# Performance work log

Hardware: AMD Instinct MI355X
Metric: run time of the kernel (lower is better)

The kernel has to match this reference:

```python
import jax, jax.numpy as jnp
import numpy as np

B, S, D = 4, 2048, 1024
H, DH = 16, 64  # dim_q = dim_k = D // H
DFF = 4096


def setup_inputs() -> dict:
    key = jax.random.key(0)
    ks = jax.random.split(key, 12)
    sd = 0.02
    x = jax.random.normal(ks[0], (B, S, D), dtype=jnp.float32)
    mask = jax.random.randint(ks[1], (B, S, S), 0, 2) == 1  # True = masked
    Wq = jax.random.normal(ks[2], (H, D, DH), dtype=jnp.float32) * sd
    bq = jnp.zeros((H, DH), dtype=jnp.float32)
    Wk = jax.random.normal(ks[3], (H, D, DH), dtype=jnp.float32) * sd
    bk = jnp.zeros((H, DH), dtype=jnp.float32)
    Wv = jax.random.normal(ks[4], (H, D, DH), dtype=jnp.float32) * sd
    bv = jnp.zeros((H, DH), dtype=jnp.float32)
    Wo = jax.random.normal(ks[5], (H * DH, D), dtype=jnp.float32) * sd
    bo = jnp.zeros((D,), dtype=jnp.float32)
    W1 = jax.random.normal(ks[6], (D, DFF), dtype=jnp.float32) * sd
    b1 = jnp.zeros((DFF,), dtype=jnp.float32)
    W2 = jax.random.normal(ks[7], (DFF, D), dtype=jnp.float32) * sd
    b2 = jnp.zeros((D,), dtype=jnp.float32)
    return dict(x=x, mask=mask, Wq=Wq, bq=bq, Wk=Wk, bk=bk, Wv=Wv, bv=bv,
                Wo=Wo, bo=bo, W1=W1, b1=b1, W2=W2, b2=b2)


def reference(x, mask, Wq, bq, Wk, bk, Wv, bv, Wo, bo, W1, b1, W2, b2):
    # x: [B,S,D]; mask: [B,S,S] bool (True -> masked)
    # Per-head projections, batched over heads: [B,H,S,DH]
    q = jnp.einsum('bsd,hde->bhse', x, Wq) + bq[None, :, None, :]
    k = jnp.einsum('bsd,hde->bhse', x, Wk) + bk[None, :, None, :]
    v = jnp.einsum('bsd,hde->bhse', x, Wv) + bv[None, :, None, :]
    # NOTE: source scales by sqrt(seq_len) (query.size(1)), reproduced faithfully.
    scale = x.shape[1] ** 0.5
    scores = jnp.einsum('bhse,bhte->bhst', q, k) / scale  # [B,H,S,S]
    scores = jnp.where(mask[:, None, :, :], -1e9, scores)
    attn = jax.nn.softmax(scores, axis=-1)
    ctx = jnp.einsum('bhst,bhte->bhse', attn, v)  # [B,H,S,DH]
    # concat heads -> [B,S,H*DH], output projection
    ctx = jnp.transpose(ctx, (0, 2, 1, 3)).reshape(x.shape[0], x.shape[1], -1)
    out = ctx @ Wo + bo
    # FFN (no residual/LayerNorm in source; dropout = identity in eval)
    h = jax.nn.relu(out @ W1 + b1)
    return h @ W2 + b2
```

## Files before the change

### kernel.cpp

```cpp
#include <hip/hip_runtime.h>
#include <hip/hip_bf16.h>


#define SDIM 2048
#define DDIM 1024

using floatx4 = __attribute__((ext_vector_type(4))) float;
using bf16x8  = __attribute__((ext_vector_type(8))) __bf16;
using bf16x4  = __attribute__((ext_vector_type(4))) __bf16;
using short4v = __attribute__((ext_vector_type(4))) short;

#define GLDS16(gptr, lptr)                                                        \
    __builtin_amdgcn_global_load_lds(                                             \
        (const __attribute__((address_space(1))) void*)(uintptr_t)(gptr),         \
        (__attribute__((address_space(3))) void*)(uintptr_t)(lptr), 16, 0, 0)


__global__ void k_f2b(const float* __restrict__ in, __bf16* __restrict__ out) {
    long i = ((long)blockIdx.x * 256 + threadIdx.x) * 4;
    float4 f = *(const float4*)(in + i);
    bf16x4 v;
    v[0] = (__bf16)f.x; v[1] = (__bf16)f.y; v[2] = (__bf16)f.z; v[3] = (__bf16)f.w;
    *(bf16x4*)(out + i) = v;
}

__global__ void k_tr(const float* __restrict__ in, __bf16* __restrict__ out, int R, int C) {
    __shared__ float t[32][33];
    int nrt = R >> 5;
    int tr = blockIdx.x % nrt, tc = blockIdx.x / nrt;
    int r0 = tr * 32, c0 = tc * 32;
    int lx = threadIdx.x & 31, ly = threadIdx.x >> 5;
    #pragma unroll
    for (int i = 0; i < 32; i += 8) t[ly + i][lx] = in[(long)(r0 + ly + i) * C + c0 + lx];
    __syncthreads();
    #pragma unroll
    for (int i = 0; i < 32; i += 8) out[(long)(c0 + ly + i) * R + r0 + lx] = (__bf16)t[lx][ly + i];
}

__global__ void k_pack_qkvw(const float* __restrict__ Wq, const float* __restrict__ Wk,
                            const float* __restrict__ Wv, __bf16* __restrict__ out) {
    int bid = blockIdx.x;
    int dht = bid & 1;
    int dt = (bid >> 1) & 31;
    int h = (bid >> 6) & 15;
    int which = bid >> 10;
    const float* W = (which == 0) ? Wq : (which == 1) ? Wk : Wv;
    __shared__ float t[32][33];
    int lx = threadIdx.x & 31, ly = threadIdx.x >> 5;
    const float* src = W + ((long)h * 1024 + dt * 32) * 64 + dht * 32;
    #pragma unroll
    for (int i = 0; i < 32; i += 8) t[ly + i][lx] = src[(ly + i) * 64 + lx];
    __syncthreads();
    __bf16* dst = out + ((long)(which * 1024 + h * 64 + dht * 32)) * 1024 + dt * 32;
    #pragma unroll
    for (int i = 0; i < 32; i += 8) dst[(long)(ly + i) * 1024 + lx] = (__bf16)t[lx][ly + i];
}

__global__ void k_pack_qkvb(const float* bq, const float* bk, const float* bv, float* out) {
    int i = blockIdx.x * 256 + threadIdx.x;
    if (i < 3072) {
        int which = i >> 10, r = i & 1023;
        const float* s = (which == 0) ? bq : (which == 1) ? bk : bv;
        out[i] = s[r];
    }
}

__global__ void k_probe(const unsigned* __restrict__ m, int* flag) {
    __shared__ int bad;
    if (threadIdx.x == 0) bad = 0;
    __syncthreads();
    int local = 0;
    for (int i = 0; i < 64; i++) {
        unsigned w = m[threadIdx.x + 256 * i];
        if (w != 0u && w != 1u && w != 0x3f800000u) local = 1;
    }
    if (local) atomicOr(&bad, 1);
    __syncthreads();
    if (threadIdx.x == 0) *flag = bad ? 0 : 1;
}

__global__ void k_pack_mask(const void* __restrict__ mask, const int* __restrict__ flag,
                            unsigned long long* __restrict__ bits) {
    long wid = ((long)blockIdx.x * 256 + threadIdx.x) >> 6;
    int lane = threadIdx.x & 63;
    long e = wid * 64 + lane;
    bool pred;
    if (*flag) pred = ((const unsigned*)mask)[e] != 0u;
    else       pred = ((const unsigned char*)mask)[e] != 0;
    unsigned long long bal = __ballot(pred);
    if (lane == 0) bits[wid] = bal;
}

__global__ void k_remap(const unsigned* __restrict__ bitsDW, unsigned* __restrict__ out) {
    int t = blockIdx.x * 256 + threadIdx.x;
    int q = t & 3, kt = (t >> 2) & 15, srow = t >> 6;
    uint4 md = *(const uint4*)(bitsDW + (long)srow * 64 + kt * 4);
    unsigned d[4] = {md.x, md.y, md.z, md.w};
    unsigned acc = 0;
    #pragma unroll
    for (int ct = 0; ct < 8; ct++) {
        unsigned nib = (d[ct >> 1] >> (((ct & 1) << 4) + q * 4)) & 0xFu;
        acc |= nib << (ct * 4);
    }
    out[t] = acc;
}

__global__ void k_trv(const __bf16* __restrict__ Vrow, __bf16* __restrict__ Vt) {
    __shared__ __bf16 t[32][72];
    int p = blockIdx.x >> 6, ts = blockIdx.x & 63;
    int tid = threadIdx.x;
    const __bf16* src = Vrow + ((long)p * 2048 + ts * 32) * 64;
    int s = tid >> 3, c = (tid & 7) * 8;
    *(bf16x8*)&t[s][c] = *(const bf16x8*)&src[s * 64 + c];
    __syncthreads();
    int dh = tid >> 2, sb = (tid & 3) * 8;
    bf16x8 w;
    #pragma unroll
    for (int j = 0; j < 8; j++) w[j] = t[sb + j][dh];
    *(bf16x8*)&Vt[((long)p * 64 + dh) * 2048 + ts * 32 + sb] = w;
}

#define QSZ 8388608L

template <int MODE>
__global__ __launch_bounds__(256, 4) void k_gemm(const __bf16* __restrict__ A,
                                                 const __bf16* __restrict__ Bt,
                                                 const float* __restrict__ bias,
                                                 void* __restrict__ Cout, int Ndim, int K) {
    __shared__ __align__(16) __bf16 As[128 * 64];
    __shared__ __align__(16) __bf16 Bs[128 * 64];
    const int tid = threadIdx.x;
    const int wave = tid >> 6, lane = tid & 63;
    const int q = lane >> 4, l16 = lane & 15;
    const int wr = wave >> 1, wc = wave & 1;
    const long bm = (long)blockIdx.x * 128;
    const long bn = (long)blockIdx.y * 128;
    floatx4 acc[4][4] = {};

    const int srow = lane >> 3;
    const int scol = (((lane & 7) - srow) & 7) * 8;
    const int r8 = l16 & 7;

    const char* apA0 = (const char*)As + (wr * 64 + l16) * 128 + ((q + r8) & 7) * 16;
    const char* apA1 = (const char*)As + (wr * 64 + l16) * 128 + ((q + 4 + r8) & 7) * 16;
    const char* apB0 = (const char*)Bs + (wc * 64 + l16) * 128 + ((q + r8) & 7) * 16;
    const char* apB1 = (const char*)Bs + (wc * 64 + l16) * 128 + ((q + 4 + r8) & 7) * 16;

    for (int k0 = 0; k0 < K; k0 += 64) {
        __syncthreads();
        #pragma unroll
        for (int c = 0; c < 4; c++) {
            int row0 = wave * 32 + c * 8;
            GLDS16(&A[(bm + row0 + srow) * K + k0 + scol], (char*)As + row0 * 128);
            GLDS16(&Bt[(bn + row0 + srow) * K + k0 + scol], (char*)Bs + row0 * 128);
        }
        __syncthreads();
        bf16x8 af[4], bfr[4];
        #pragma unroll
        for (int i = 0; i < 4; i++) af[i] = *(const bf16x8*)(apA0 + i * 2048);
        #pragma unroll
        for (int j = 0; j < 4; j++) bfr[j] = *(const bf16x8*)(apB0 + j * 2048);
        #pragma unroll
        for (int i = 0; i < 4; i++)
            #pragma unroll
            for (int j = 0; j < 4; j++)
                acc[i][j] = __builtin_amdgcn_mfma_f32_16x16x32_bf16(af[i], bfr[j], acc[i][j], 0, 0, 0);
        #pragma unroll
        for (int i = 0; i < 4; i++) af[i] = *(const bf16x8*)(apA1 + i * 2048);
        #pragma unroll
        for (int j = 0; j < 4; j++) bfr[j] = *(const bf16x8*)(apB1 + j * 2048);
        #pragma unroll
        for (int i = 0; i < 4; i++)
            #pragma unroll
            for (int j = 0; j < 4; j++)
                acc[i][j] = __builtin_amdgcn_mfma_f32_16x16x32_bf16(af[i], bfr[j], acc[i][j], 0, 0, 0);
    }

    const int mrow0 = (int)bm + wr * 64 + q * 4;
    const int ncol0 = (int)bn + wc * 64;
    #pragma unroll
    for (int j = 0; j < 4; j++) {
        int nbase = ncol0 + j * 16 + l16;
        float bv = bias[nbase];
        #pragma unroll
        for (int i = 0; i < 4; i++) {
            #pragma unroll
            for (int r = 0; r < 4; r++) {
                int mm = mrow0 + i * 16 + r;
                float v = acc[i][j][r] + bv;
                if (MODE == 2) v = fmaxf(v, 0.f);
                if (MODE == 3) {
                    ((float*)Cout)[(long)mm * Ndim + nbase] = v;
                } else if (MODE == 0) {
                    int which = nbase >> 10, rem = nbase & 1023;
                    int hh = rem >> 6, dh = rem & 63;
                    int bb = mm >> 11, ss = mm & 2047;
                    long pr = (long)(bb * 16 + hh);
                    __bf16* o = (__bf16*)Cout;
                    if (which == 0) {
                        v *= 0.03188152837f;
                        o[(pr * 2048 + ss) * 64 + dh] = (__bf16)v;
                    } else if (which == 1) o[QSZ + (pr * 2048 + ss) * 64 + dh] = (__bf16)v;
                    else o[3 * QSZ + (pr * 2048 + ss) * 64 + dh] = (__bf16)v;
                } else {
                    ((__bf16*)Cout)[(long)mm * Ndim + nbase] = (__bf16)v;
                }
            }
        }
    }
}

__global__ __launch_bounds__(256, 3) void k_attn(const __bf16* __restrict__ Q,
                                                 const __bf16* __restrict__ Kb,
                                                 const __bf16* __restrict__ Vt,
                                                 const unsigned* __restrict__ bitw2,
                                                 __bf16* __restrict__ ctx) {
    __shared__ __align__(16) __bf16 Qs[128 * 64];
    __shared__ __align__(16) __bf16 Ks[128 * 64];
    __shared__ __align__(16) __bf16 Vts[64 * 128];
    const int tid = threadIdx.x, wave = tid >> 6, lane = tid & 63;
    const int q = lane >> 4, l16 = lane & 15;
    const int pair = blockIdx.x & 63, qt = blockIdx.x >> 6;
    const int b = pair >> 4, h = pair & 15;

    const int srow8 = lane >> 3;
    const int scol8 = (((lane & 7) - srow8) & 7) * 8;
    const int r8 = l16 & 7;
    const int vrow = lane >> 4;
    const int vl = lane & 15;

    const __bf16* Qp = Q + ((long)pair * SDIM + qt * 128) * 64;
    #pragma unroll
    for (int c = 0; c < 4; c++) {
        int row0 = wave * 32 + c * 8;
        GLDS16(&Qp[(row0 + srow8) * 64 + scol8], (char*)Qs + row0 * 128);
    }
    __syncthreads();
    bf16x8 qf[2][2];
    #pragma unroll
    for (int g = 0; g < 2; g++) {
        const char* qb = (const char*)Qs + (wave * 32 + g * 16 + l16) * 128;
        qf[g][0] = *(const bf16x8*)(qb + ((q + r8) & 7) * 16);
        qf[g][1] = *(const bf16x8*)(qb + ((q + 4 + r8) & 7) * 16);
    }

    const char* kp0 = (const char*)Ks + l16 * 128 + ((q + r8) & 7) * 16;
    const char* kp1 = (const char*)Ks + l16 * 128 + ((q + 4 + r8) & 7) * 16;
    const char* vp[8];
    #pragma unroll
    for (int ct = 0; ct < 8; ct++)
        vp[ct] = (const char*)Vts + l16 * 256 + (q & 1) * 8 + ((ct * 2 + (q >> 1) + l16) & 15) * 16;
    const int qrow = qt * 128 + wave * 32 + l16;
    const unsigned* mp0 = bitw2 + ((long)(b * SDIM + qrow)) * 64 + q;
    const unsigned* mp1 = mp0 + 16 * 64;

    floatx4 o[2][4] = {};
    floatx4 o5[2] = {};
    short4v ones;
    { union { unsigned u[2]; short4v s; } c; c.u[0] = 0x3F803F80u; c.u[1] = 0x3F803F80u; ones = c.s; }

    for (int kt = 0; kt < 16; kt++) {
        __syncthreads();
        const __bf16* Kp = Kb + ((long)pair * SDIM + kt * 128) * 64;
        #pragma unroll
        for (int c = 0; c < 4; c++) {
            int row0 = wave * 32 + c * 8;
            GLDS16(&Kp[(row0 + srow8) * 64 + scol8], (char*)Ks + row0 * 128);
        }
        const __bf16* Vp = Vt + ((long)pair * 64) * SDIM + kt * 128;
        #pragma unroll
        for (int c = 0; c < 4; c++) {
            int row0 = wave * 16 + c * 4;
            int gsrc = ((vl - (c * 4 + vrow)) & 15) * 8;
            GLDS16(&Vp[(long)(row0 + vrow) * SDIM + gsrc], (char*)Vts + row0 * 256);
        }
        const unsigned w32a = mp0[kt * 4];
        const unsigned w32b = mp1[kt * 4];
        __syncthreads();

        __builtin_amdgcn_s_setprio(1);
        floatx4 st0[8], st1[8];
        #pragma unroll
        for (int ct = 0; ct < 8; ct++) {
            bf16x8 kf0 = *(const bf16x8*)(kp0 + ct * 2048);
            bf16x8 kf1 = *(const bf16x8*)(kp1 + ct * 2048);
            floatx4 z0 = {}, z1 = {};
            z0 = __builtin_amdgcn_mfma_f32_16x16x32_bf16(kf0, qf[0][0], z0, 0, 0, 0);
            z1 = __builtin_amdgcn_mfma_f32_16x16x32_bf16(kf0, qf[1][0], z1, 0, 0, 0);
            z0 = __builtin_amdgcn_mfma_f32_16x16x32_bf16(kf1, qf[0][1], z0, 0, 0, 0);
            z1 = __builtin_amdgcn_mfma_f32_16x16x32_bf16(kf1, qf[1][1], z1, 0, 0, 0);
            st0[ct] = z0; st1[ct] = z1;
        }
        #pragma unroll
        for (int ct = 0; ct < 8; ct++) {
            union { unsigned u[2]; short4v s; } pu0, pu1;
            {
                float p0 = __builtin_amdgcn_exp2f(st0[ct][0]);
                float p1 = __builtin_amdgcn_exp2f(st0[ct][1]);
                float p2 = __builtin_amdgcn_exp2f(st0[ct][2]);
                float p3 = __builtin_amdgcn_exp2f(st0[ct][3]);
                p0 = (w32a & (1u << (ct * 4 + 0))) ? 0.f : p0;
                p1 = (w32a & (1u << (ct * 4 + 1))) ? 0.f : p1;
                p2 = (w32a & (1u << (ct * 4 + 2))) ? 0.f : p2;
                p3 = (w32a & (1u << (ct * 4 + 3))) ? 0.f : p3;
                union { float f; unsigned u; } c0, c1, c2, c3;
                c0.f = p0; c1.f = p1; c2.f = p2; c3.f = p3;
                pu0.u[0] = __builtin_amdgcn_perm(c1.u, c0.u, 0x07060302u);
                pu0.u[1] = __builtin_amdgcn_perm(c3.u, c2.u, 0x07060302u);
            }
            {
                float p0 = __builtin_amdgcn_exp2f(st1[ct][0]);
                float p1 = __builtin_amdgcn_exp2f(st1[ct][1]);
                float p2 = __builtin_amdgcn_exp2f(st1[ct][2]);
                float p3 = __builtin_amdgcn_exp2f(st1[ct][3]);
                p0 = (w32b & (1u << (ct * 4 + 0))) ? 0.f : p0;
                p1 = (w32b & (1u << (ct * 4 + 1))) ? 0.f : p1;
                p2 = (w32b & (1u << (ct * 4 + 2))) ? 0.f : p2;
                p3 = (w32b & (1u << (ct * 4 + 3))) ? 0.f : p3;
                union { float f; unsigned u; } c0, c1, c2, c3;
                c0.f = p0; c1.f = p1; c2.f = p2; c3.f = p3;
                pu1.u[0] = __builtin_amdgcn_perm(c1.u, c0.u, 0x07060302u);
                pu1.u[1] = __builtin_amdgcn_perm(c3.u, c2.u, 0x07060302u);
            }
            #pragma unroll
            for (int d = 0; d < 4; d++) {
                union { bf16x4 b; short4v s; } vu;
                vu.b = *(const bf16x4*)(vp[ct] + d * 4096);
                o[0][d] = __builtin_amdgcn_mfma_f32_16x16x16bf16_1k(vu.s, pu0.s, o[0][d], 0, 0, 0);
                o[1][d] = __builtin_amdgcn_mfma_f32_16x16x16bf16_1k(vu.s, pu1.s, o[1][d], 0, 0, 0);
            }
            o5[0] = __builtin_amdgcn_mfma_f32_16x16x16bf16_1k(ones, pu0.s, o5[0], 0, 0, 0);
            o5[1] = __builtin_amdgcn_mfma_f32_16x16x16bf16_1k(ones, pu1.s, o5[1], 0, 0, 0);
        }
        __builtin_amdgcn_s_setprio(0);
    }
    #pragma unroll
    for (int g = 0; g < 2; g++) {
        float inv = 1.0f / o5[g][0];
        long base = ((long)b * SDIM + qrow + g * 16) * DDIM + h * 64;
        #pragma unroll
        for (int d = 0; d < 4; d++) {
            bf16x4 w;
            #pragma unroll
            for (int r = 0; r < 4; r++) w[r] = (__bf16)(o[g][d][r] * inv);
            *(bf16x4*)&ctx[base + d * 16 + q * 4] = w;
        }
    }
}


extern "C" void kernel_launch(void* const* d_in, const int* in_sizes, int n_in,
                              void* d_out, int out_size, void* d_ws, size_t ws_size,
                              hipStream_t stream) {
    const float* x = (const float*)d_in[0];
    const void* mask = d_in[1];
    const float* Wq = (const float*)d_in[2];
    const float* bq = (const float*)d_in[3];
    const float* Wk = (const float*)d_in[4];
    const float* bk = (const float*)d_in[5];
    const float* Wv = (const float*)d_in[6];
    const float* bv = (const float*)d_in[7];
    const float* Wo = (const float*)d_in[8];
    const float* bo = (const float*)d_in[9];
    const float* W1 = (const float*)d_in[10];
    const float* b1 = (const float*)d_in[11];
    const float* W2 = (const float*)d_in[12];
    const float* b2 = (const float*)d_in[13];

    char* ws = (char*)d_ws;
    __bf16* xb   = (__bf16*)(ws + 0);
    __bf16* Qb   = (__bf16*)(ws + 16777216);
    __bf16* Kb   = (__bf16*)(ws + 33554432);
    __bf16* Vtb  = (__bf16*)(ws + 50331648);
    __bf16* Vrow = (__bf16*)(ws + 67108864);
    __bf16* hbuf = (__bf16*)(ws + 33554432);
    __bf16* wqkvt = (__bf16*)(ws + 100663296);
    __bf16* wot  = (__bf16*)(ws + 106954752);
    __bf16* w1t  = (__bf16*)(ws + 109051904);
    __bf16* w2t  = (__bf16*)(ws + 117440512);
    float* bqkv  = (float*)(ws + 125829120);
    int* flag    = (int*)(ws + 125841408);
    __bf16* ctx = xb;
    __bf16* attn_out = Qb;
    unsigned long long* bits = (unsigned long long*)wqkvt;
    unsigned* bits2 = (unsigned*)((char*)wqkvt + 2097152);
    (void)Vrow;

    k_f2b<<<8192, 256, 0, stream>>>(x, xb);
    k_pack_qkvw<<<3072, 256, 0, stream>>>(Wq, Wk, Wv, wqkvt);
    k_pack_qkvb<<<12, 256, 0, stream>>>(bq, bk, bv, bqkv);
    k_tr<<<1024, 256, 0, stream>>>(Wo, wot, 1024, 1024);
    k_tr<<<4096, 256, 0, stream>>>(W1, w1t, 1024, 4096);
    k_tr<<<4096, 256, 0, stream>>>(W2, w2t, 4096, 1024);
    k_probe<<<1, 256, 0, stream>>>((const unsigned*)mask, flag);

    {
        dim3 g(64, 24);
        k_gemm<0><<<g, 256, 0, stream>>>(xb, wqkvt, bqkv, (void*)Qb, 3072, 1024);
    }
    k_trv<<<4096, 256, 0, stream>>>(Vrow, Vtb);
    k_pack_mask<<<65536, 256, 0, stream>>>(mask, flag, bits);
    k_remap<<<2048, 256, 0, stream>>>((const unsigned*)bits, bits2);
    k_attn<<<1024, 256, 0, stream>>>(Qb, Kb, Vtb, bits2, ctx);
    {
        dim3 g(64, 8);
        k_gemm<1><<<g, 256, 0, stream>>>(ctx, wot, bo, (void*)attn_out, 1024, 1024);
    }
    {
        dim3 g(64, 32);
        k_gemm<2><<<g, 256, 0, stream>>>(attn_out, w1t, b1, (void*)hbuf, 4096, 1024);
    }
    {
        dim3 g(64, 8);
        k_gemm<3><<<g, 256, 0, stream>>>(hbuf, w2t, b2, d_out, 1024, 4096);
    }
}
```

Measured before the change: 595.7 us.

## Double-buffer K/V tiles in attention kernel to overlap loads with compute

The attention kernel now uses two LDS buffers for K and V^T and prefetches the next key tile while computing on the current one. Explicit vmcnt waits and barriers replace the per-iteration syncthreads pairs. The mask bitword layout is remapped so each lane reads contiguous words indexed by kt. Launch bounds drop from 3 to 2 blocks per CU because LDS use grows, which trades occupancy for load/compute overlap.

```diff
diff --git a/kernel.cpp b/kernel.cpp
--- a/kernel.cpp
+++ b/kernel.cpp
@@ -102,7 +102,7 @@
         unsigned nib = (d[ct >> 1] >> (((ct & 1) << 4) + q * 4)) & 0xFu;
         acc |= nib << (ct * 4);
     }
-    out[t] = acc;
+    out[srow * 64 + q * 16 + kt] = acc;
 }
 
 __global__ void k_trv(const __bf16* __restrict__ Vrow, __bf16* __restrict__ Vt) {
@@ -210,14 +210,14 @@
     }
 }
 
-__global__ __launch_bounds__(256, 3) void k_attn(const __bf16* __restrict__ Q,
+__global__ __launch_bounds__(256, 2) void k_attn(const __bf16* __restrict__ Q,
                                                  const __bf16* __restrict__ Kb,
                                                  const __bf16* __restrict__ Vt,
                                                  const unsigned* __restrict__ bitw2,
                                                  __bf16* __restrict__ ctx) {
     __shared__ __align__(16) __bf16 Qs[128 * 64];
-    __shared__ __align__(16) __bf16 Ks[128 * 64];
-    __shared__ __align__(16) __bf16 Vts[64 * 128];
+    __shared__ __align__(16) __bf16 Ks[2][128 * 64];
+    __shared__ __align__(16) __bf16 Vts[2][64 * 128];
     const int tid = threadIdx.x, wave = tid >> 6, lane = tid & 63;
     const int q = lane >> 4, l16 = lane & 15;
     const int pair = blockIdx.x & 63, qt = blockIdx.x >> 6;
@@ -229,13 +229,47 @@
     const int vrow = lane >> 4;
     const int vl = lane & 15;
 
+    const char* kp0 = (const char*)Ks + l16 * 128 + ((q + r8) & 7) * 16;
+    const char* kp1 = (const char*)Ks + l16 * 128 + ((q + 4 + r8) & 7) * 16;
+    const char* vp[8];
+    #pragma unroll
+    for (int ct = 0; ct < 8; ct++)
+        vp[ct] = (const char*)Vts + l16 * 256 + (q & 1) * 8 + ((ct * 2 + (q >> 1) + l16) & 15) * 16;
+    const int qrow = qt * 128 + wave * 32 + l16;
+    const unsigned* mp0 = bitw2 + ((long)(b * SDIM + qrow)) * 64 + q * 16;
+    const unsigned* mp1 = mp0 + 16 * 64;
+
+    floatx4 o[2][4] = {};
+    floatx4 o5[2] = {};
+    short4v ones;
+    { union { unsigned u[2]; short4v s; } c; c.u[0] = 0x3F803F80u; c.u[1] = 0x3F803F80u; ones = c.s; }
+
+    auto stage_kv = [&](int kt, int bufsel) __attribute__((always_inline)) {
+        const __bf16* Kp = Kb + ((long)pair * SDIM + kt * 128) * 64;
+        #pragma unroll
+        for (int c = 0; c < 4; c++) {
+            int row0 = wave * 32 + c * 8;
+            GLDS16(&Kp[(row0 + srow8) * 64 + scol8], (char*)Ks + bufsel * 16384 + row0 * 128);
+        }
+        const __bf16* Vp = Vt + ((long)pair * 64) * SDIM + kt * 128;
+        #pragma unroll
+        for (int c = 0; c < 4; c++) {
+            int row0 = wave * 16 + c * 4;
+            int gsrc = ((vl - (c * 4 + vrow)) & 15) * 8;
+            GLDS16(&Vp[(long)(row0 + vrow) * SDIM + gsrc], (char*)Vts + bufsel * 16384 + row0 * 256);
+        }
+    };
+
     const __bf16* Qp = Q + ((long)pair * SDIM + qt * 128) * 64;
     #pragma unroll
     for (int c = 0; c < 4; c++) {
         int row0 = wave * 32 + c * 8;
         GLDS16(&Qp[(row0 + srow8) * 64 + scol8], (char*)Qs + row0 * 128);
     }
-    __syncthreads();
+    unsigned waA = mp0[0], wbA = mp1[0];
+    stage_kv(0, 0);
+    asm volatile("s_waitcnt vmcnt(8)\n\ts_barrier" ::: "memory");
+
     bf16x8 qf[2][2];
     #pragma unroll
     for (int g = 0; g < 2; g++) {
@@ -244,46 +278,13 @@
         qf[g][1] = *(const bf16x8*)(qb + ((q + 4 + r8) & 7) * 16);
     }
 
-    const char* kp0 = (const char*)Ks + l16 * 128 + ((q + r8) & 7) * 16;
-    const char* kp1 = (const char*)Ks + l16 * 128 + ((q + 4 + r8) & 7) * 16;
-    const char* vp[8];
-    #pragma unroll
-    for (int ct = 0; ct < 8; ct++)
-        vp[ct] = (const char*)Vts + l16 * 256 + (q & 1) * 8 + ((ct * 2 + (q >> 1) + l16) & 15) * 16;
-    const int qrow = qt * 128 + wave * 32 + l16;
-    const unsigned* mp0 = bitw2 + ((long)(b * SDIM + qrow)) * 64 + q;
-    const unsigned* mp1 = mp0 + 16 * 64;
-
-    floatx4 o[2][4] = {};
-    floatx4 o5[2] = {};
-    short4v ones;
-    { union { unsigned u[2]; short4v s; } c; c.u[0] = 0x3F803F80u; c.u[1] = 0x3F803F80u; ones = c.s; }
-
-    for (int kt = 0; kt < 16; kt++) {
-        __syncthreads();
-        const __bf16* Kp = Kb + ((long)pair * SDIM + kt * 128) * 64;
-        #pragma unroll
-        for (int c = 0; c < 4; c++) {
-            int row0 = wave * 32 + c * 8;
-            GLDS16(&Kp[(row0 + srow8) * 64 + scol8], (char*)Ks + row0 * 128);
-        }
-        const __bf16* Vp = Vt + ((long)pair * 64) * SDIM + kt * 128;
-        #pragma unroll
-        for (int c = 0; c < 4; c++) {
-            int row0 = wave * 16 + c * 4;
-            int gsrc = ((vl - (c * 4 + vrow)) & 15) * 8;
-            GLDS16(&Vp[(long)(row0 + vrow) * SDIM + gsrc], (char*)Vts + row0 * 256);
-        }
-        const unsigned w32a = mp0[kt * 4];
-        const unsigned w32b = mp1[kt * 4];
-        __syncthreads();
-
+    auto compute = [&](int off, unsigned w32a, unsigned w32b) __attribute__((always_inline)) {
         __builtin_amdgcn_s_setprio(1);
         floatx4 st0[8], st1[8];
         #pragma unroll
         for (int ct = 0; ct < 8; ct++) {
-            bf16x8 kf0 = *(const bf16x8*)(kp0 + ct * 2048);
-            bf16x8 kf1 = *(const bf16x8*)(kp1 + ct * 2048);
+            bf16x8 kf0 = *(const bf16x8*)(kp0 + off + ct * 2048);
+            bf16x8 kf1 = *(const bf16x8*)(kp1 + off + ct * 2048);
             floatx4 z0 = {}, z1 = {};
             z0 = __builtin_amdgcn_mfma_f32_16x16x32_bf16(kf0, qf[0][0], z0, 0, 0, 0);
             z1 = __builtin_amdgcn_mfma_f32_16x16x32_bf16(kf0, qf[1][0], z1, 0, 0, 0);
@@ -325,7 +326,7 @@
             #pragma unroll
             for (int d = 0; d < 4; d++) {
                 union { bf16x4 b; short4v s; } vu;
-                vu.b = *(const bf16x4*)(vp[ct] + d * 4096);
+                vu.b = *(const bf16x4*)(vp[ct] + off + d * 4096);
                 o[0][d] = __builtin_amdgcn_mfma_f32_16x16x16bf16_1k(vu.s, pu0.s, o[0][d], 0, 0, 0);
                 o[1][d] = __builtin_amdgcn_mfma_f32_16x16x16bf16_1k(vu.s, pu1.s, o[1][d], 0, 0, 0);
             }
@@ -333,7 +334,31 @@
             o5[1] = __builtin_amdgcn_mfma_f32_16x16x16bf16_1k(ones, pu1.s, o5[1], 0, 0, 0);
         }
         __builtin_amdgcn_s_setprio(0);
-    }
+    };
+
+    #pragma unroll 1
+    for (int kt = 0; kt < 14; kt += 2) {
+        unsigned waB = mp0[kt + 1], wbB = mp1[kt + 1];
+        stage_kv(kt + 1, 1);
+        asm volatile("s_waitcnt vmcnt(10)\n\ts_barrier" ::: "memory");
+        compute(0, waA, wbA);
+        asm volatile("s_barrier" ::: "memory");
+        waA = mp0[kt + 2]; wbA = mp1[kt + 2];
+        stage_kv(kt + 2, 0);
+        asm volatile("s_waitcnt vmcnt(10)\n\ts_barrier" ::: "memory");
+        compute(16384, waB, wbB);
+        asm volatile("s_barrier" ::: "memory");
+    }
+    {
+        unsigned waB = mp0[15], wbB = mp1[15];
+        stage_kv(15, 1);
+        asm volatile("s_waitcnt vmcnt(10)\n\ts_barrier" ::: "memory");
+        compute(0, waA, wbA);
+        asm volatile("s_barrier" ::: "memory");
+        asm volatile("s_waitcnt vmcnt(0)\n\ts_barrier" ::: "memory");
+        compute(16384, waB, wbB);
+    }
+
     #pragma unroll
     for (int g = 0; g < 2; g++) {
         float inv = 1.0f / o5[g][0];
```

After: 592.0 us (median of 2 runs). No clear change (-0.6%).
